# Kernel tuning notes

Measured on AMD Instinct MI355X. Metric: run time of the kernel, lower is better.

The kernel has to match this reference:

```python
import jax, jax.numpy as jnp
import numpy as np

N = 8192   # nodes per graph
F = 128    # input feature dim
H = 512    # GAT hidden dim
D = 256    # GAT output dim (== match_size, required by matching broadcast)
MS = 256   # match_size
E = 131072 # edges per graph (one direction)
EPS = 1e-8 # torch cosine_similarity eps


def _xavier(k, shape):
    lim = (6.0 / (shape[0] + shape[-1])) ** 0.5
    return jax.random.uniform(k, shape, jnp.float32, -lim, lim)


def setup_inputs() -> dict:
    key = jax.random.key(0)
    ks = jax.random.split(key, 24)
    return {
        "x_s": jax.random.normal(ks[0], (N, F), jnp.float32),
        "x_t": jax.random.normal(ks[1], (N, F), jnp.float32),
        "edge_index_s": jax.random.randint(ks[2], (2, E), 0, N),
        "edge_index_t": jax.random.randint(ks[3], (2, E), 0, N),
        "label": jax.random.randint(ks[4], (1,), 0, 2),
        # GAT params (2 single-head layers)
        "W_g1": _xavier(ks[5], (F, H)),
        "a1_src": _xavier(ks[6], (H, 1))[:, 0],
        "a1_dst": _xavier(ks[7], (H, 1))[:, 0],
        "W_g2": _xavier(ks[8], (H, D)),
        "a2_src": _xavier(ks[9], (D, 1))[:, 0],
        "a2_dst": _xavier(ks[10], (D, 1))[:, 0],
        # readout_rep
        "W_read": _xavier(ks[11], (D, D)),
        # matching
        "W_match": _xavier(ks[12], (D, MS)),
        # MLP
        "mlp_w1": _xavier(ks[13], (MS * 8, MS * 2)), "mlp_b1": jnp.zeros((MS * 2,), jnp.float32),
        "mlp_w2": _xavier(ks[14], (MS * 2, MS)),     "mlp_b2": jnp.zeros((MS,), jnp.float32),
        "mlp_w3": _xavier(ks[15], (MS, MS // 2)),    "mlp_b3": jnp.zeros((MS // 2,), jnp.float32),
        "mlp_w4": _xavier(ks[16], (MS // 2, 1)),     "mlp_b4": jnp.zeros((1,), jnp.float32),
    }


def _gat_layer(h_in, src, dst, W, a_s, a_d, n):
    h = h_in @ W                                           # [n, d_out]
    logits = (h[src] * a_s).sum(-1) + (h[dst] * a_d).sum(-1)
    e = jax.nn.leaky_relu(logits, 0.2)
    m = jax.ops.segment_max(e, dst, num_segments=n)
    ex = jnp.exp(e - m[dst])
    den = jax.ops.segment_sum(ex, dst, num_segments=n)
    alpha = ex / (den[dst] + 1e-16)
    return jax.ops.segment_sum(alpha[:, None] * h[src], dst, num_segments=n)


def _gat(x, edge_index, W1, a1s, a1d, W2, a2s, a2d):
    n = x.shape[0]
    sl = jnp.arange(n)
    # symmetrize undirected edge list + add self loops (PyG GATConv convention)
    src = jnp.concatenate([edge_index[0], edge_index[1], sl])
    dst = jnp.concatenate([edge_index[1], edge_index[0], sl])
    h = jax.nn.elu(_gat_layer(x, src, dst, W1, a1s, a1d, n))
    return _gat_layer(h, src, dst, W2, a2s, a2d, n)


def _readout(h, W):
    g = jnp.tanh(jnp.mean(h, 0) @ W)                       # [d]
    s = jax.nn.sigmoid(h @ g)                              # [n]
    return (s[:, None] * h).sum(0, keepdims=True)          # [1, d]


def _match(h1, h2, Wm):
    # cosine over feature dim of (h * W) without materializing [N, D, MS]:
    # dot[n,m] = sum_d h1[n,d]*W[d,m]*h2[n,d]*W[d,m] = ((h1*h2) @ W^2)[n,m]
    W2 = Wm * Wm
    dot = (h1 * h2) @ W2
    n1 = jnp.sqrt((h1 * h1) @ W2)
    n2 = jnp.sqrt((h2 * h2) @ W2)
    return dot / jnp.maximum(n1 * n2, EPS)


def _mutual(h1, h2):
    n1 = jnp.linalg.norm(h1, axis=-1)
    n2 = jnp.linalg.norm(h2, axis=-1)
    cos = (h1 @ h2.T) / jnp.maximum(n1[:, None] * n2[None, :], EPS)  # [N, M]
    coe = cos / cos.sum(0)                                 # column-normalize
    return coe @ h2


def _mlp(z, w1, b1, w2, b2, w3, b3, w4, b4):
    z = jax.nn.relu(z @ w1 + b1)
    z = jax.nn.relu(z @ w2 + b2)
    z = jax.nn.relu(z @ w3 + b3)
    return jax.nn.sigmoid(z @ w4 + b4)


def _forward(x_s, x_t, edge_index_s, edge_index_t, label,
             W_g1, a1_src, a1_dst, W_g2, a2_src, a2_dst,
             W_read, W_match,
             mlp_w1, mlp_b1, mlp_w2, mlp_b2, mlp_w3, mlp_b3, mlp_w4, mlp_b4):
    f1 = (x_s - jnp.mean(x_s)) / jnp.std(x_s, ddof=1)
    f2 = (x_t - jnp.mean(x_t)) / jnp.std(x_t, ddof=1)

    h1 = _gat(f1, edge_index_s, W_g1, a1_src, a1_dst, W_g2, a2_src, a2_dst)
    h2 = _gat(f2, edge_index_t, W_g1, a1_src, a1_dst, W_g2, a2_src, a2_dst)

    h1g = _readout(h1, W_read)
    h2g = _readout(h2, W_read)

    h1m = _mutual(h1, h2)
    h2m = _mutual(h2, h1)
    h1mg = _readout(h1m, W_read)
    h2mg = _readout(h2m, W_read)

    miu1 = _match(h1, h1m, W_match); miu2 = _match(h2, h2m, W_match)
    miu1g = _readout(miu1, W_read);  miu2g = _readout(miu2, W_read)
    phi1 = _match(h1, h1mg, W_match); phi2 = _match(h2, h2mg, W_match)
    phi1g = _readout(phi1, W_read);   phi2g = _readout(phi2, W_read)
    psi1 = _match(h1g, h1m, W_match); psi2 = _match(h2g, h2m, W_match)
    psi1g = _readout(psi1, W_read);   psi2g = _readout(psi2, W_read)
    om1 = _match(h1g, h1mg, W_match); om2 = _match(h2g, h2mg, W_match)

    z1 = jnp.concatenate([miu1g, phi1g, psi1g, om1], axis=1).T  # [4*MS, 1]
    z2 = jnp.concatenate([miu2g, phi2g, psi2g, om2], axis=1).T
    z = jnp.concatenate([z1, z2], axis=0).T                     # [1, 8*MS]
    z = _mlp(z, mlp_w1, mlp_b1, mlp_w2, mlp_b2, mlp_w3, mlp_b3, mlp_w4, mlp_b4)
    return z


def reference(x_s, x_t, edge_index_s, edge_index_t, label,
              W_g1, a1_src, a1_dst, W_g2, a2_src, a2_dst,
              W_read, W_match,
              mlp_w1, mlp_b1, mlp_w2, mlp_b2, mlp_w3, mlp_b3, mlp_w4, mlp_b4):
    z = _forward(x_s, x_t, edge_index_s, edge_index_t, label,
                 W_g1, a1_src, a1_dst, W_g2, a2_src, a2_dst, W_read, W_match,
                 mlp_w1, mlp_b1, mlp_w2, mlp_b2, mlp_w3, mlp_b3, mlp_w4, mlp_b4)
    label_exp = jnp.exp(-label.astype(jnp.float32))
    return z, label, label_exp
```

## Files before the change

kernel.cpp:

```cpp
#include <hip/hip_runtime.h>
#include <hip/hip_bf16.h>
#include <math.h>
#include <stddef.h>

#define NN 8192
#define FF 128
#define HH 512
#define DDIM 256
#define EE 131072
#define ET (2*EE + NN)
#define FEPS 1e-8f

typedef float f32x4 __attribute__((ext_vector_type(4)));
typedef __bf16 bf16x8 __attribute__((ext_vector_type(8)));
typedef unsigned short u16;

static __device__ __forceinline__ u16 f2bf(float f) {
  union { float f; unsigned u; } v; v.f = f;
  return (u16)((v.u + 0x7fffu + ((v.u >> 16) & 1u)) >> 16);
}
static __device__ __forceinline__ float bf2f(u16 h) {
  union { unsigned u; float f; } v; v.u = ((unsigned)h) << 16;
  return v.f;
}
static __device__ __forceinline__ f32x4 mfma16(bf16x8 a, bf16x8 b, f32x4 c) {
  return __builtin_amdgcn_mfma_f32_16x16x32_bf16(a, b, c, 0, 0, 0);
}

struct PLB { const u16* p[6]; int slot[6]; };

__global__ void k_reduce2(const float* __restrict__ xa, const float* __restrict__ xb,
                          int n, double* __restrict__ out) {
  const float* x = blockIdx.y ? xb : xa;
  double* o = out + 2 * blockIdx.y;
  __shared__ double s1[256], s2[256];
  double a = 0.0, b = 0.0;
  for (int i = blockIdx.x * blockDim.x + threadIdx.x; i < n; i += gridDim.x * blockDim.x) {
    double v = (double)x[i];
    a += v; b += v * v;
  }
  s1[threadIdx.x] = a; s2[threadIdx.x] = b;
  __syncthreads();
  for (int w = 128; w > 0; w >>= 1) {
    if (threadIdx.x < w) { s1[threadIdx.x] += s1[threadIdx.x + w]; s2[threadIdx.x] += s2[threadIdx.x + w]; }
    __syncthreads();
  }
  if (threadIdx.x == 0) { atomicAdd(&o[0], s1[0]); atomicAdd(&o[1], s2[0]); }
}

__global__ void k_normalize2(const float* __restrict__ xa, const float* __restrict__ xb,
                             u16* __restrict__ ya, u16* __restrict__ yb, int n,
                             const double* __restrict__ s) {
  const float* x = blockIdx.y ? xb : xa;
  u16* y = blockIdx.y ? yb : ya;
  const double* sp = s + 2 * blockIdx.y;
  double mean = sp[0] / (double)n;
  double var = (sp[1] - (double)n * mean * mean) / (double)(n - 1);
  float mu = (float)mean;
  float inv = (float)(1.0 / sqrt(var));
  for (int i = blockIdx.x * blockDim.x + threadIdx.x; i < n; i += gridDim.x * blockDim.x)
    y[i] = f2bf((x[i] - mu) * inv);
}

__global__ void k_hist(const int* __restrict__ ei, int* __restrict__ deg) {
  int t = blockIdx.x * blockDim.x + threadIdx.x;
  if (t >= ET) return;
  int dst = (t < EE) ? ei[EE + t] : ((t < 2*EE) ? ei[t - EE] : (t - 2*EE));
  atomicAdd(&deg[dst], 1);
}

__global__ void k_scan(const int* __restrict__ deg, int* __restrict__ offs, int* __restrict__ cursor) {
  __shared__ int ts[256];
  int tid = threadIdx.x;
  int loc[32];
  int s = 0;
  #pragma unroll
  for (int i = 0; i < 32; ++i) { loc[i] = s; s += deg[tid * 32 + i]; }
  ts[tid] = s;
  __syncthreads();
  for (int off = 1; off < 256; off <<= 1) {
    int v = (tid >= off) ? ts[tid - off] : 0;
    __syncthreads();
    ts[tid] += v;
    __syncthreads();
  }
  int pre = ts[tid] - s;
  #pragma unroll
  for (int i = 0; i < 32; ++i) {
    int o = pre + loc[i];
    offs[tid * 32 + i] = o;
    cursor[tid * 32 + i] = o;
  }
  if (tid == 255) offs[NN] = ts[255];
}

__global__ void k_scatter(const int* __restrict__ ei, int* __restrict__ cursor, int* __restrict__ srcs) {
  int t = blockIdx.x * blockDim.x + threadIdx.x;
  if (t >= ET) return;
  int src = (t < 2*EE) ? ei[t] : (t - 2*EE);
  int dst = (t < EE) ? ei[EE + t] : ((t < 2*EE) ? ei[t - EE] : (t - 2*EE));
  int pos = atomicAdd(&cursor[dst], 1);
  srcs[pos] = src;
}

__global__ __launch_bounds__(256) void k_tr_bf16(const float* __restrict__ src, u16* __restrict__ dst,
                                                 int R, int C, int sq) {
  __shared__ float T[32][33];
  int tx = threadIdx.x & 31, ty = threadIdx.x >> 5;
  int r0 = blockIdx.y * 32, c0 = blockIdx.x * 32;
  #pragma unroll
  for (int p = 0; p < 4; ++p)
    T[ty + 8 * p][tx] = src[(size_t)(r0 + ty + 8 * p) * C + c0 + tx];
  __syncthreads();
  #pragma unroll
  for (int p = 0; p < 4; ++p) {
    float v = T[tx][ty + 8 * p];
    if (sq) v *= v;
    dst[(size_t)(c0 + ty + 8 * p) * R + r0 + tx] = f2bf(v);
  }
}

__global__ __launch_bounds__(256) void k_tr2w(const float* __restrict__ hA, const float* __restrict__ scA,
                                              u16* __restrict__ tA, u16* __restrict__ wA,
                                              const float* __restrict__ hB, const float* __restrict__ scB,
                                              u16* __restrict__ tB, u16* __restrict__ wB) {
  __shared__ float T[32][33];
  __shared__ float W[32][33];
  const float* src = blockIdx.z ? hB : hA;
  const float* sc  = blockIdx.z ? scB : scA;
  u16* dt = blockIdx.z ? tB : tA;
  u16* dw = blockIdx.z ? wB : wA;
  int tx = threadIdx.x & 31, ty = threadIdx.x >> 5;
  int r0 = blockIdx.y * 32, c0 = blockIdx.x * 32;
  #pragma unroll
  for (int p = 0; p < 4; ++p) {
    int j = r0 + ty + 8 * p;
    float v = src[(size_t)j * DDIM + c0 + tx];
    T[ty + 8 * p][tx] = v;
    W[ty + 8 * p][tx] = v * sc[j];
  }
  __syncthreads();
  #pragma unroll
  for (int p = 0; p < 4; ++p) {
    size_t o = (size_t)(c0 + ty + 8 * p) * NN + r0 + tx;
    dt[o] = f2bf(T[tx][ty + 8 * p]);
    dw[o] = f2bf(W[tx][ty + 8 * p]);
  }
}

__global__ __launch_bounds__(256) void k_gemm_bf(const u16* __restrict__ A, const u16* __restrict__ Bt,
                                                 u16* __restrict__ Cb, int K, int N,
                                                 const float* __restrict__ as_, const float* __restrict__ ad_,
                                                 float* __restrict__ hs, float* __restrict__ hd) {
  int w = threadIdx.x >> 6, l = threadIdx.x & 63, r15 = l & 15, g = l >> 4;
  int i0 = blockIdx.y * 64 + w * 16;
  int n0 = blockIdx.x * 128;
  f32x4 zero = {0.f, 0.f, 0.f, 0.f};
  f32x4 acc[8];
  #pragma unroll
  for (int n = 0; n < 8; ++n) acc[n] = zero;
  int kcN = K >> 5;
  const u16* arow = A + (size_t)(i0 + r15) * K + g * 8;
  for (int kc = 0; kc < kcN; ++kc) {
    bf16x8 a = *reinterpret_cast<const bf16x8*>(arow + kc * 32);
    #pragma unroll
    for (int n = 0; n < 8; ++n) {
      bf16x8 b = *reinterpret_cast<const bf16x8*>(Bt + (size_t)(n0 + n * 16 + r15) * K + kc * 32 + g * 8);
      acc[n] = mfma16(a, b, acc[n]);
    }
  }
  int io = i0 + g * 4;
  #pragma unroll
  for (int n = 0; n < 8; ++n) {
    int c = n0 + n * 16 + r15;
    #pragma unroll
    for (int q = 0; q < 4; ++q)
      Cb[(size_t)(io + q) * N + c] = f2bf(acc[n][q]);
  }
  if (as_) {
    float hsum[4] = {0.f, 0.f, 0.f, 0.f}, dsum[4] = {0.f, 0.f, 0.f, 0.f};
    #pragma unroll
    for (int n = 0; n < 8; ++n) {
      int c = n0 + n * 16 + r15;
      float av = as_[c], dv = ad_[c];
      #pragma unroll
      for (int q = 0; q < 4; ++q) { hsum[q] += acc[n][q] * av; dsum[q] += acc[n][q] * dv; }
    }
    #pragma unroll
    for (int q = 0; q < 4; ++q) {
      #pragma unroll
      for (int o = 1; o < 16; o <<= 1) { hsum[q] += __shfl_xor(hsum[q], o); dsum[q] += __shfl_xor(dsum[q], o); }
    }
    if (r15 == 0) {
      #pragma unroll
      for (int q = 0; q < 4; ++q) {
        atomicAdd(&hs[io + q], hsum[q]);
        atomicAdd(&hd[io + q], dsum[q]);
      }
    }
  }
}

__global__ void k_alpha(const int* __restrict__ offs, const int* __restrict__ srcs,
                        const float* __restrict__ hs, const float* __restrict__ hd,
                        float* __restrict__ alpha) {
  int wid = (blockIdx.x * blockDim.x + threadIdx.x) >> 6;
  int lane = threadIdx.x & 63;
  if (wid >= NN) return;
  int b = offs[wid], e = offs[wid + 1];
  float hdn = hd[wid];
  float m = -3.4e38f;
  for (int p = b + lane; p < e; p += 64) {
    float v = hs[srcs[p]] + hdn;
    v = v > 0.f ? v : 0.2f * v;
    alpha[p] = v;
    m = fmaxf(m, v);
  }
  #pragma unroll
  for (int o = 32; o > 0; o >>= 1) m = fmaxf(m, __shfl_xor(m, o));
  float den = 0.f;
  for (int p = b + lane; p < e; p += 64) {
    float ex = expf(alpha[p] - m);
    alpha[p] = ex;
    den += ex;
  }
  #pragma unroll
  for (int o = 32; o > 0; o >>= 1) den += __shfl_xor(den, o);
  float sc = 1.f / (den + 1e-16f);
  for (int p = b + lane; p < e; p += 64) alpha[p] *= sc;
}

__global__ __launch_bounds__(256) void k_agg3(const int* __restrict__ offs, const int* __restrict__ srcs,
                                              const float* __restrict__ alpha, const u16* __restrict__ Hb,
                                              float* __restrict__ outF, u16* __restrict__ outB,
                                              int D, int elu) {
  int wv = threadIdx.x >> 6, lane = threadIdx.x & 63;
  int n = blockIdx.x * 4 + wv;
  int b = offs[n], e = offs[n + 1];
  if (D == 512) {
    float acc[8];
    #pragma unroll
    for (int j = 0; j < 8; ++j) acc[j] = 0.f;
    const u16* base = Hb + lane * 8;
    for (int p = b; p < e; ++p) {
      float a = alpha[p];
      uint4 v = *reinterpret_cast<const uint4*>(base + (size_t)srcs[p] * 512);
      acc[0] += a * bf2f((u16)(v.x & 0xffff)); acc[1] += a * bf2f((u16)(v.x >> 16));
      acc[2] += a * bf2f((u16)(v.y & 0xffff)); acc[3] += a * bf2f((u16)(v.y >> 16));
      acc[4] += a * bf2f((u16)(v.z & 0xffff)); acc[5] += a * bf2f((u16)(v.z >> 16));
      acc[6] += a * bf2f((u16)(v.w & 0xffff)); acc[7] += a * bf2f((u16)(v.w >> 16));
    }
    ushort4 o0, o1;
    #pragma unroll
    for (int j = 0; j < 8; ++j)
      if (elu) acc[j] = acc[j] > 0.f ? acc[j] : (expf(acc[j]) - 1.f);
    o0.x = f2bf(acc[0]); o0.y = f2bf(acc[1]); o0.z = f2bf(acc[2]); o0.w = f2bf(acc[3]);
    o1.x = f2bf(acc[4]); o1.y = f2bf(acc[5]); o1.z = f2bf(acc[6]); o1.w = f2bf(acc[7]);
    u16* ob = outB + (size_t)n * 512 + lane * 8;
    *reinterpret_cast<ushort4*>(ob) = o0;
    *reinterpret_cast<ushort4*>(ob + 4) = o1;
  } else {
    float acc[4];
    #pragma unroll
    for (int j = 0; j < 4; ++j) acc[j] = 0.f;
    const u16* base = Hb + lane * 4;
    for (int p = b; p < e; ++p) {
      float a = alpha[p];
      uint2 v = *reinterpret_cast<const uint2*>(base + (size_t)srcs[p] * 256);
      acc[0] += a * bf2f((u16)(v.x & 0xffff)); acc[1] += a * bf2f((u16)(v.x >> 16));
      acc[2] += a * bf2f((u16)(v.y & 0xffff)); acc[3] += a * bf2f((u16)(v.y >> 16));
    }
    #pragma unroll
    for (int j = 0; j < 4; ++j)
      if (elu) acc[j] = acc[j] > 0.f ? acc[j] : (expf(acc[j]) - 1.f);
    if (outF) {
      float4 of = {acc[0], acc[1], acc[2], acc[3]};
      *reinterpret_cast<float4*>(outF + (size_t)n * 256 + lane * 4) = of;
    }
    ushort4 ob;
    ob.x = f2bf(acc[0]); ob.y = f2bf(acc[1]); ob.z = f2bf(acc[2]); ob.w = f2bf(acc[3]);
    *reinterpret_cast<ushort4*>(outB + (size_t)n * 256 + lane * 4) = ob;
  }
}

__global__ void k_rninv2(const float* __restrict__ h1, const float* __restrict__ h2,
                         float* __restrict__ o1, float* __restrict__ o2) {
  const float* h = blockIdx.y ? h2 : h1;
  float* o = blockIdx.y ? o2 : o1;
  int wid = (blockIdx.x * blockDim.x + threadIdx.x) >> 6;
  int lane = threadIdx.x & 63;
  if (wid >= NN) return;
  float4 v = *reinterpret_cast<const float4*>(h + (size_t)wid * DDIM + lane * 4);
  float a = v.x * v.x + v.y * v.y + v.z * v.z + v.w * v.w;
  #pragma unroll
  for (int o2_ = 32; o2_ > 0; o2_ >>= 1) a += __shfl_xor(a, o2_);
  if (!lane) o[wid] = 1.f / sqrtf(a);
}

__global__ void k_wsum(const float* __restrict__ h1, const float* __restrict__ h2,
                       const float* __restrict__ n1inv, const float* __restrict__ n2inv,
                       float* __restrict__ ut) {
  const float* h = blockIdx.y ? h2 : h1;
  const float* wv = blockIdx.y ? n2inv : n1inv;
  float* o = ut + 256 * blockIdx.y;
  int d = threadIdx.x;
  int r0 = blockIdx.x * 128;
  float acc = 0.f;
  for (int r = 0; r < 128; ++r) acc += wv[r0 + r] * h[(size_t)(r0 + r) * 256 + d];
  atomicAdd(&o[d], acc);
}

__global__ void k_rs(const float* __restrict__ h1, const float* __restrict__ h2,
                     const float* __restrict__ n1inv, const float* __restrict__ n2inv,
                     const float* __restrict__ ut, float* __restrict__ R, float* __restrict__ S) {
  const float* h  = blockIdx.y ? h2 : h1;
  const float* ni = blockIdx.y ? n2inv : n1inv;
  const float* gv = blockIdx.y ? ut : ut + 256;
  float* o = blockIdx.y ? S : R;
  int wid = (blockIdx.x * blockDim.x + threadIdx.x) >> 6;
  int lane = threadIdx.x & 63;
  if (wid >= NN) return;
  float4 v = *reinterpret_cast<const float4*>(h + (size_t)wid * 256 + lane * 4);
  float4 g4 = *reinterpret_cast<const float4*>(gv + lane * 4);
  float a = v.x * g4.x + v.y * g4.y + v.z * g4.z + v.w * g4.w;
  #pragma unroll
  for (int o2_ = 32; o2_ > 0; o2_ >>= 1) a += __shfl_xor(a, o2_);
  if (!lane) o[wid] = ni[wid] * a;
}

__global__ void k_scj(const float* __restrict__ S, const float* __restrict__ R,
                      const float* __restrict__ n1inv, const float* __restrict__ n2inv,
                      float* __restrict__ scj1, float* __restrict__ scj2) {
  int j = blockIdx.x * blockDim.x + threadIdx.x;
  if (j >= NN) return;
  scj1[j] = n2inv[j] / S[j];
  scj2[j] = n1inv[j] / R[j];
}

__global__ __launch_bounds__(256) void k_gemm_M(const u16* __restrict__ A1, const u16* __restrict__ B1,
                                                const u16* __restrict__ A2, const u16* __restrict__ B2,
                                                float* __restrict__ Mf) {
  int mat = blockIdx.z & 1, kch = blockIdx.z >> 1;
  const u16* A = mat ? A2 : A1;
  const u16* Bt = mat ? B2 : B1;
  float* C = Mf + mat * 65536;
  int w = threadIdx.x >> 6, l = threadIdx.x & 63, r15 = l & 15, g = l >> 4;
  int i0 = blockIdx.y * 64 + w * 16;
  int n0 = blockIdx.x * 128;
  f32x4 zero = {0.f, 0.f, 0.f, 0.f};
  f32x4 acc[8];
  #pragma unroll
  for (int n = 0; n < 8; ++n) acc[n] = zero;
  const u16* arow = A + (size_t)(i0 + r15) * NN + g * 8;
  for (int kc = kch * 16; kc < kch * 16 + 16; ++kc) {
    bf16x8 a = *reinterpret_cast<const bf16x8*>(arow + kc * 32);
    #pragma unroll
    for (int n = 0; n < 8; ++n) {
      bf16x8 b = *reinterpret_cast<const bf16x8*>(Bt + (size_t)(n0 + n * 16 + r15) * NN + kc * 32 + g * 8);
      acc[n] = mfma16(a, b, acc[n]);
    }
  }
  int io = i0 + g * 4;
  #pragma unroll
  for (int n = 0; n < 8; ++n) {
    int c = n0 + n * 16 + r15;
    #pragma unroll
    for (int q = 0; q < 4; ++q)
      atomicAdd(&C[(size_t)(io + q) * 256 + c], acc[n][q]);
  }
}

__global__ void k_m2bf(const float* __restrict__ Mf, u16* __restrict__ Mb) {
  size_t o = (size_t)blockIdx.y * 65536 + blockIdx.x * 256 + threadIdx.x;
  Mb[o] = f2bf(Mf[o]);
}

__global__ __launch_bounds__(256) void k_gemm_hm(const u16* __restrict__ A1, const u16* __restrict__ M1,
                                                 const float* __restrict__ s1, u16* __restrict__ O1,
                                                 const u16* __restrict__ A2, const u16* __restrict__ M2,
                                                 const float* __restrict__ s2, u16* __restrict__ O2) {
  int z = blockIdx.z;
  const u16* A = z ? A2 : A1;
  const u16* Bt = z ? M2 : M1;
  const float* sc = z ? s2 : s1;
  u16* O = z ? O2 : O1;
  int w = threadIdx.x >> 6, l = threadIdx.x & 63, r15 = l & 15, g = l >> 4;
  int i0 = blockIdx.y * 64 + w * 16;
  int n0 = blockIdx.x * 128;
  f32x4 zero = {0.f, 0.f, 0.f, 0.f};
  f32x4 acc[8];
  #pragma unroll
  for (int n = 0; n < 8; ++n) acc[n] = zero;
  const u16* arow = A + (size_t)(i0 + r15) * 256 + g * 8;
  #pragma unroll
  for (int kc = 0; kc < 8; ++kc) {
    bf16x8 a = *reinterpret_cast<const bf16x8*>(arow + kc * 32);
    #pragma unroll
    for (int n = 0; n < 8; ++n) {
      bf16x8 b = *reinterpret_cast<const bf16x8*>(Bt + (size_t)(n0 + n * 16 + r15) * 256 + kc * 32 + g * 8);
      acc[n] = mfma16(a, b, acc[n]);
    }
  }
  int io = i0 + g * 4;
  float s4[4];
  #pragma unroll
  for (int q = 0; q < 4; ++q) s4[q] = sc[io + q];
  #pragma unroll
  for (int n = 0; n < 8; ++n) {
    int c = n0 + n * 16 + r15;
    #pragma unroll
    for (int q = 0; q < 4; ++q)
      O[(size_t)(io + q) * 256 + c] = f2bf(acc[n][q] * s4[q]);
  }
}

__global__ void k_w2d(const u16* __restrict__ W2t, const float* __restrict__ ogs,
                      u16* __restrict__ W2d, float* __restrict__ yn) {
  __shared__ float red[256];
  int n = blockIdx.x, z = blockIdx.y, k = threadIdx.x;
  int map = (z == 0) ? 512 : (z == 1) ? 0 : (z == 2) ? 768 : 256;
  float y = ogs[map + k];
  float wv = bf2f(W2t[n * 256 + k]);
  W2d[z * 65536 + n * 256 + k] = f2bf(wv * y);
  red[k] = wv * y * y;
  __syncthreads();
  for (int s = 128; s > 0; s >>= 1) {
    if (k < s) red[k] += red[k + s];
    __syncthreads();
  }
  if (!k) yn[z * 256 + n] = rsqrtf(fmaxf(red[0], 1e-30f));
}

__global__ __launch_bounds__(256) void k_match5(
    const u16* __restrict__ h1b, const u16* __restrict__ h1mb,
    const u16* __restrict__ h2b, const u16* __restrict__ h2mb,
    const u16* __restrict__ W2t, const u16* __restrict__ W2dB, const float* __restrict__ ynB,
    u16* __restrict__ mb0, u16* __restrict__ mb1, u16* __restrict__ mb2,
    u16* __restrict__ mb3, u16* __restrict__ mb4, u16* __restrict__ mb5) {
  int z = blockIdx.z;
  const u16* A  = z ? h2b : h1b;
  const u16* Am = z ? h2mb : h1mb;
  const u16* Wphi = W2dB + (size_t)(z ? 2 : 0) * 65536;
  const u16* Wpsi = W2dB + (size_t)(z ? 3 : 1) * 65536;
  const float* ynphi = ynB + (z ? 512 : 0);
  const float* ynpsi = ynB + (z ? 768 : 256);
  u16* oMiu = z ? mb3 : mb0;
  u16* oPhi = z ? mb4 : mb1;
  u16* oPsi = z ? mb5 : mb2;
  int w = threadIdx.x >> 6, l = threadIdx.x & 63, r15 = l & 15, g = l >> 4;
  int i0 = blockIdx.y * 64 + w * 16;
  int n0 = blockIdx.x * 64;
  f32x4 zero = {0.f, 0.f, 0.f, 0.f};
  f32x4 aP[4], aQ[4], aU[4], aD1[4], aD2[4];
  #pragma unroll
  for (int n = 0; n < 4; ++n) { aP[n] = zero; aQ[n] = zero; aU[n] = zero; aD1[n] = zero; aD2[n] = zero; }
  size_t abase = (size_t)(i0 + r15) * 256 + g * 8;
  #pragma unroll 2
  for (int kc = 0; kc < 8; ++kc) {
    uint4 xa = *reinterpret_cast<const uint4*>(A + abase + kc * 32);
    uint4 xc = *reinterpret_cast<const uint4*>(Am + abase + kc * 32);
    bf16x8 fa = *reinterpret_cast<const bf16x8*>(&xa);
    bf16x8 fc = *reinterpret_cast<const bf16x8*>(&xc);
    bf16x8 fu, fp, fq;
    float ta, tc;
    ta = bf2f((u16)(xa.x & 0xffff)); tc = bf2f((u16)(xc.x & 0xffff));
    fu[0] = (__bf16)(ta * tc); fp[0] = (__bf16)(ta * ta); fq[0] = (__bf16)(tc * tc);
    ta = bf2f((u16)(xa.x >> 16));    tc = bf2f((u16)(xc.x >> 16));
    fu[1] = (__bf16)(ta * tc); fp[1] = (__bf16)(ta * ta); fq[1] = (__bf16)(tc * tc);
    ta = bf2f((u16)(xa.y & 0xffff)); tc = bf2f((u16)(xc.y & 0xffff));
    fu[2] = (__bf16)(ta * tc); fp[2] = (__bf16)(ta * ta); fq[2] = (__bf16)(tc * tc);
    ta = bf2f((u16)(xa.y >> 16));    tc = bf2f((u16)(xc.y >> 16));
    fu[3] = (__bf16)(ta * tc); fp[3] = (__bf16)(ta * ta); fq[3] = (__bf16)(tc * tc);
    ta = bf2f((u16)(xa.z & 0xffff)); tc = bf2f((u16)(xc.z & 0xffff));
    fu[4] = (__bf16)(ta * tc); fp[4] = (__bf16)(ta * ta); fq[4] = (__bf16)(tc * tc);
    ta = bf2f((u16)(xa.z >> 16));    tc = bf2f((u16)(xc.z >> 16));
    fu[5] = (__bf16)(ta * tc); fp[5] = (__bf16)(ta * ta); fq[5] = (__bf16)(tc * tc);
    ta = bf2f((u16)(xa.w & 0xffff)); tc = bf2f((u16)(xc.w & 0xffff));
    fu[6] = (__bf16)(ta * tc); fp[6] = (__bf16)(ta * ta); fq[6] = (__bf16)(tc * tc);
    ta = bf2f((u16)(xa.w >> 16));    tc = bf2f((u16)(xc.w >> 16));
    fu[7] = (__bf16)(ta * tc); fp[7] = (__bf16)(ta * ta); fq[7] = (__bf16)(tc * tc);
    #pragma unroll
    for (int n = 0; n < 4; ++n) {
      size_t boff = (size_t)(n0 + n * 16 + r15) * 256 + kc * 32 + g * 8;
      bf16x8 bw = *reinterpret_cast<const bf16x8*>(W2t + boff);
      aP[n] = mfma16(fp, bw, aP[n]);
      aQ[n] = mfma16(fq, bw, aQ[n]);
      aU[n] = mfma16(fu, bw, aU[n]);
      bf16x8 b1 = *reinterpret_cast<const bf16x8*>(Wphi + boff);
      aD1[n] = mfma16(fa, b1, aD1[n]);
      bf16x8 b2 = *reinterpret_cast<const bf16x8*>(Wpsi + boff);
      aD2[n] = mfma16(fc, b2, aD2[n]);
    }
  }
  int io = i0 + g * 4;
  #pragma unroll
  for (int n = 0; n < 4; ++n) {
    int c = n0 + n * 16 + r15;
    float y1 = ynphi[c], y2 = ynpsi[c];
    #pragma unroll
    for (int q = 0; q < 4; ++q) {
      float rp = rsqrtf(fmaxf(aP[n][q], 1e-30f));
      float rq = rsqrtf(fmaxf(aQ[n][q], 1e-30f));
      size_t idx = (size_t)(io + q) * 256 + c;
      oMiu[idx] = f2bf(aU[n][q] * rp * rq);
      oPhi[idx] = f2bf(aD1[n][q] * rp * y1);
      oPsi[idx] = f2bf(aD2[n][q] * rq * y2);
    }
  }
}

__global__ void k_match_g(const float* __restrict__ X1, const float* __restrict__ Y1,
                          const float* __restrict__ X2, const float* __restrict__ Y2,
                          const float* __restrict__ W2, float* __restrict__ v) {
  __shared__ float u[256], p[256], q[256];
  const float* X = blockIdx.x ? X2 : X1;
  const float* Y = blockIdx.x ? Y2 : Y1;
  float* o = v + (blockIdx.x ? 1792 : 768);
  int t = threadIdx.x;
  float xv = X[t], yv = Y[t];
  u[t] = xv * yv; p[t] = xv * xv; q[t] = yv * yv;
  __syncthreads();
  float a = 0.f, b = 0.f, c = 0.f;
  #pragma unroll 4
  for (int d = 0; d < 256; ++d) {
    float wv = W2[(size_t)d * DDIM + t];
    a += u[d] * wv; b += p[d] * wv; c += q[d] * wv;
  }
  o[t] = a / fmaxf(sqrtf(b) * sqrtf(c), FEPS);
}

__global__ void k_w2(const float* __restrict__ Wm, float* __restrict__ W2, int n) {
  int i = blockIdx.x * blockDim.x + threadIdx.x;
  if (i < n) { float v = Wm[i]; W2[i] = v * v; }
}

__global__ void k_bmu_b(PLB L, float* __restrict__ mu) {
  const u16* h = L.p[blockIdx.y];
  int d = threadIdx.x;
  int r0 = blockIdx.x * 128;
  float acc = 0.f;
  for (int r = 0; r < 128; ++r) acc += bf2f(h[(size_t)(r0 + r) * 256 + d]);
  atomicAdd(&mu[blockIdx.y * 256 + d], acc);
}

__global__ void k_bgv(const float* __restrict__ mu, const float* __restrict__ Wr,
                      float* __restrict__ g) {
  __shared__ float ls[256];
  int m = blockIdx.x, t = threadIdx.x;
  ls[t] = mu[m * 256 + t] * (1.f / (float)NN);
  __syncthreads();
  float acc = 0.f;
  #pragma unroll 4
  for (int d = 0; d < 256; ++d) acc += ls[d] * Wr[(size_t)d * 256 + t];
  g[m * 256 + t] = tanhf(acc);
}

__global__ __launch_bounds__(256) void k_bsc_b(PLB L, const float* __restrict__ g,
                                               float* __restrict__ v) {
  __shared__ __align__(16) float gs[256];
  __shared__ float sarr[32];
  int m = blockIdx.y;
  const u16* h = L.p[m];
  int t = threadIdx.x, w = t >> 6, l = t & 63;
  gs[t] = g[m * 256 + t];
  __syncthreads();
  int r0 = blockIdx.x * 32;
  float4 gv4 = reinterpret_cast<const float4*>(gs)[l];
  for (int rr = w * 8; rr < w * 8 + 8; ++rr) {
    ushort4 hv = *reinterpret_cast<const ushort4*>(h + (size_t)(r0 + rr) * 256 + l * 4);
    float dot = bf2f(hv.x) * gv4.x + bf2f(hv.y) * gv4.y + bf2f(hv.z) * gv4.z + bf2f(hv.w) * gv4.w;
    #pragma unroll
    for (int o = 32; o > 0; o >>= 1) dot += __shfl_xor(dot, o);
    if (!l) sarr[rr] = 1.f / (1.f + expf(-dot));
  }
  __syncthreads();
  float acc = 0.f;
  for (int rr = 0; rr < 32; ++rr) acc += sarr[rr] * bf2f(h[(size_t)(r0 + rr) * 256 + t]);
  atomicAdd(&v[L.slot[m] + t], acc);
}

__global__ void k_binit(const float* __restrict__ b1, const float* __restrict__ b2,
                        const float* __restrict__ b3, float* __restrict__ l1,
                        float* __restrict__ l2, float* __restrict__ l3) {
  int t = blockIdx.x * 256 + threadIdx.x;
  if (t < 512) l1[t] = b1[t];
  if (t < 256) l2[t] = b2[t];
  if (t < 128) l3[t] = b3[t];
}

__global__ void k_gemv(const float* __restrict__ vin, const float* __restrict__ w,
                       float* __restrict__ out, int K, int M, int Kc, int relu_in) {
  int m = blockIdx.x * 256 + threadIdx.x;
  if (m >= M) return;
  int k0 = blockIdx.y * Kc;
  float acc = 0.f;
  #pragma unroll 4
  for (int k = k0; k < k0 + Kc; ++k) {
    float x = vin[k];
    if (relu_in) x = fmaxf(x, 0.f);
    acc += x * w[(size_t)k * M + m];
  }
  atomicAdd(&out[m], acc);
}

__global__ void k_final(const float* __restrict__ l3, const float* __restrict__ w4,
                        const float* __restrict__ b4, const int* __restrict__ label,
                        float* __restrict__ out) {
  __shared__ float ls[128];
  int t = threadIdx.x;
  ls[t] = fmaxf(l3[t], 0.f) * w4[t];
  __syncthreads();
  for (int w = 64; w > 0; w >>= 1) { if (t < w) ls[t] += ls[t + w]; __syncthreads(); }
  if (t == 0) {
    float z = 1.f / (1.f + expf(-(ls[0] + b4[0])));
    out[0] = z;
    float lb = (float)label[0];
    out[1] = lb;
    out[2] = expf(-lb);
  }
}

extern "C" void kernel_launch(void* const* d_in, const int* in_sizes, int n_in,
                              void* d_out, int out_size, void* d_ws, size_t ws_size,
                              hipStream_t stream) {
  (void)in_sizes; (void)n_in; (void)out_size;
  const float* x_s   = (const float*)d_in[0];
  const float* x_t   = (const float*)d_in[1];
  const int*   ei_s  = (const int*)d_in[2];
  const int*   ei_t  = (const int*)d_in[3];
  const int*   label = (const int*)d_in[4];
  const float* W_g1  = (const float*)d_in[5];
  const float* a1s   = (const float*)d_in[6];
  const float* a1d   = (const float*)d_in[7];
  const float* W_g2  = (const float*)d_in[8];
  const float* a2s   = (const float*)d_in[9];
  const float* a2d   = (const float*)d_in[10];
  const float* W_read  = (const float*)d_in[11];
  const float* W_match = (const float*)d_in[12];
  const float* w1 = (const float*)d_in[13]; const float* b1 = (const float*)d_in[14];
  const float* w2 = (const float*)d_in[15]; const float* b2 = (const float*)d_in[16];
  const float* w3 = (const float*)d_in[17]; const float* b3 = (const float*)d_in[18];
  const float* w4 = (const float*)d_in[19]; const float* b4 = (const float*)d_in[20];
  float* out = (float*)d_out;

  char* base = (char*)d_ws;
  size_t off = 0;
  auto alloc = [&](size_t bytes) -> void* {
    void* pp = base + off;
    off = (off + bytes + 255) & ~(size_t)255;
    return pp;
  };
  double* dsum = (double*)alloc(4 * sizeof(double));
  u16*   hb_bf= (u16*)alloc((size_t)NN * HH * 2);
  u16*   aggb = (u16*)alloc((size_t)NN * HH * 2);
  float* h1   = (float*)alloc((size_t)NN * DDIM * 4);
  float* h2   = (float*)alloc((size_t)NN * DDIM * 4);
  u16*   f1b  = (u16*)alloc((size_t)NN * FF * 2);
  u16*   f2b  = (u16*)alloc((size_t)NN * FF * 2);
  u16*   h1b  = (u16*)alloc((size_t)NN * DDIM * 2);
  u16*   h2b  = (u16*)alloc((size_t)NN * DDIM * 2);
  u16*   h1mb = (u16*)alloc((size_t)NN * DDIM * 2);
  u16*   h2mb = (u16*)alloc((size_t)NN * DDIM * 2);
  u16*   h1t  = (u16*)alloc((size_t)NN * DDIM * 2);
  u16*   h2t  = (u16*)alloc((size_t)NN * DDIM * 2);
  u16*   wh1t = (u16*)alloc((size_t)NN * DDIM * 2);
  u16*   wh2t = (u16*)alloc((size_t)NN * DDIM * 2);
  u16*   mb0  = (u16*)alloc((size_t)NN * DDIM * 2);
  u16*   mb1  = (u16*)alloc((size_t)NN * DDIM * 2);
  u16*   mb2  = (u16*)alloc((size_t)NN * DDIM * 2);
  u16*   mb3  = (u16*)alloc((size_t)NN * DDIM * 2);
  u16*   mb4  = (u16*)alloc((size_t)NN * DDIM * 2);
  u16*   mb5  = (u16*)alloc((size_t)NN * DDIM * 2);
  float* alpha= (float*)alloc((size_t)ET * 4);
  int*   srcs = (int*)alloc((size_t)ET * 4);
  int*   deg  = (int*)alloc(NN * 4);
  int*   curs = (int*)alloc(NN * 4);
  int*   offs = (int*)alloc((NN + 1) * 4);
  float* n1inv= (float*)alloc(NN * 4);
  float* n2inv= (float*)alloc(NN * 4);
  float* Rr   = (float*)alloc(NN * 4);
  float* Ss   = (float*)alloc(NN * 4);
  float* scj1 = (float*)alloc(NN * 4);
  float* scj2 = (float*)alloc(NN * 4);
  float* hsb  = (float*)alloc(NN * 4);
  float* hdb  = (float*)alloc(NN * 4);
  float* W2   = (float*)alloc((size_t)DDIM * DDIM * 4);
  u16*   Wg1t = (u16*)alloc((size_t)HH * FF * 2);
  u16*   Wg2t = (u16*)alloc((size_t)DDIM * HH * 2);
  u16*   W2t  = (u16*)alloc((size_t)DDIM * DDIM * 2);
  u16*   W2dB = (u16*)alloc(4 * 65536 * 2);
  float* ynB  = (float*)alloc(4 * 256 * 4);
  u16*   Mb   = (u16*)alloc(2 * 65536 * 2);
  float* mug1 = (float*)alloc(4 * 256 * 4);
  float* ogs  = (float*)alloc(4 * 256 * 4);
  float* mug2 = (float*)alloc(6 * 256 * 4);
  float* v    = (float*)alloc(2048 * 4);
  float* ut   = (float*)alloc(512 * 4);
  float* Mf   = (float*)alloc(2 * 65536 * 4);
  float* g1   = (float*)alloc(4 * 256 * 4);
  float* g2   = (float*)alloc(6 * 256 * 4);
  float* l1o  = (float*)alloc(512 * 4);
  float* l2o  = (float*)alloc(256 * 4);
  float* l3o  = (float*)alloc(128 * 4);
  if (off > ws_size) return;

  float* h1g  = ogs + 0;
  float* h2g  = ogs + 256;
  float* h1mg = ogs + 512;
  float* h2mg = ogs + 768;
  const size_t zr_bytes = (4 * 256 + 4 * 256 + 6 * 256 + 2048 + 512 + 2 * 65536) * 4;

  hipMemsetAsync(dsum, 0, 4 * sizeof(double), stream);
  k_reduce2<<<dim3(1024, 2), 256, 0, stream>>>(x_s, x_t, NN * FF, dsum);
  k_normalize2<<<dim3(1024, 2), 256, 0, stream>>>(x_s, x_t, f1b, f2b, NN * FF, dsum);

  k_tr_bf16<<<dim3(HH / 32, FF / 32), 256, 0, stream>>>(W_g1, Wg1t, FF, HH, 0);
  k_tr_bf16<<<dim3(DDIM / 32, HH / 32), 256, 0, stream>>>(W_g2, Wg2t, HH, DDIM, 0);
  k_tr_bf16<<<dim3(DDIM / 32, DDIM / 32), 256, 0, stream>>>(W_match, W2t, DDIM, DDIM, 1);
  k_w2<<<dim3((DDIM * DDIM + 255) / 256), 256, 0, stream>>>(W_match, W2, DDIM * DDIM);

  auto run_gat = [&](const u16* finb, const int* ei, float* hout, u16* houtb) {
    hipMemsetAsync(deg, 0, NN * 4, stream);
    k_hist<<<dim3((ET + 255) / 256), 256, 0, stream>>>(ei, deg);
    k_scan<<<1, 256, 0, stream>>>(deg, offs, curs);
    k_scatter<<<dim3((ET + 255) / 256), 256, 0, stream>>>(ei, curs, srcs);
    hipMemsetAsync(hsb, 0, 2 * NN * 4, stream);
    k_gemm_bf<<<dim3(HH / 128, NN / 64), 256, 0, stream>>>(finb, Wg1t, hb_bf, FF, HH, a1s, a1d, hsb, hdb);
    k_alpha<<<dim3(NN / 4), 256, 0, stream>>>(offs, srcs, hsb, hdb, alpha);
    k_agg3<<<dim3(NN / 4), 256, 0, stream>>>(offs, srcs, alpha, hb_bf, nullptr, aggb, HH, 1);
    hipMemsetAsync(hsb, 0, 2 * NN * 4, stream);
    k_gemm_bf<<<dim3(DDIM / 128, NN / 64), 256, 0, stream>>>(aggb, Wg2t, hb_bf, HH, DDIM, a2s, a2d, hsb, hdb);
    k_alpha<<<dim3(NN / 4), 256, 0, stream>>>(offs, srcs, hsb, hdb, alpha);
    k_agg3<<<dim3(NN / 4), 256, 0, stream>>>(offs, srcs, alpha, hb_bf, hout, houtb, DDIM, 0);
  };
  run_gat(f1b, ei_s, h1, h1b);
  run_gat(f2b, ei_t, h2, h2b);

  k_rninv2<<<dim3(NN / 4, 2), 256, 0, stream>>>(h1, h2, n1inv, n2inv);
  hipMemsetAsync(mug1, 0, zr_bytes, stream);
  k_wsum<<<dim3(64, 2), 256, 0, stream>>>(h1, h2, n1inv, n2inv, ut);
  k_rs<<<dim3(NN / 4, 2), 256, 0, stream>>>(h1, h2, n1inv, n2inv, ut, Rr, Ss);
  k_scj<<<dim3(NN / 256), 256, 0, stream>>>(Ss, Rr, n1inv, n2inv, scj1, scj2);
  k_tr2w<<<dim3(DDIM / 32, NN / 32, 2), 256, 0, stream>>>(h2, scj1, h2t, wh2t, h1, scj2, h1t, wh1t);
  k_gemm_M<<<dim3(2, 4, 32), 256, 0, stream>>>(wh2t, h2t, wh1t, h1t, Mf);
  k_m2bf<<<dim3(256, 2), 256, 0, stream>>>(Mf, Mb);
  k_gemm_hm<<<dim3(2, 128, 2), 256, 0, stream>>>(h1b, Mb, n1inv, h1mb,
                                                 h2b, Mb + 65536, n2inv, h2mb);

  PLB g1l;
  g1l.p[0] = h1b;  g1l.slot[0] = 0;
  g1l.p[1] = h2b;  g1l.slot[1] = 256;
  g1l.p[2] = h1mb; g1l.slot[2] = 512;
  g1l.p[3] = h2mb; g1l.slot[3] = 768;
  k_bmu_b<<<dim3(64, 4), 256, 0, stream>>>(g1l, mug1);
  k_bgv<<<dim3(4), 256, 0, stream>>>(mug1, W_read, g1);
  k_bsc_b<<<dim3(256, 4), 256, 0, stream>>>(g1l, g1, ogs);

  k_w2d<<<dim3(256, 4), 256, 0, stream>>>(W2t, ogs, W2dB, ynB);
  k_match5<<<dim3(4, 128, 2), 256, 0, stream>>>(h1b, h1mb, h2b, h2mb, W2t, W2dB, ynB,
                                                mb0, mb1, mb2, mb3, mb4, mb5);
  k_match_g<<<dim3(2), 256, 0, stream>>>(h1g, h1mg, h2g, h2mg, W2, v);

  PLB g2l;
  g2l.p[0] = mb0; g2l.slot[0] = 0;
  g2l.p[1] = mb1; g2l.slot[1] = 256;
  g2l.p[2] = mb2; g2l.slot[2] = 512;
  g2l.p[3] = mb3; g2l.slot[3] = 1024;
  g2l.p[4] = mb4; g2l.slot[4] = 1280;
  g2l.p[5] = mb5; g2l.slot[5] = 1536;
  k_bmu_b<<<dim3(64, 6), 256, 0, stream>>>(g2l, mug2);
  k_bgv<<<dim3(6), 256, 0, stream>>>(mug2, W_read, g2);
  k_bsc_b<<<dim3(256, 6), 256, 0, stream>>>(g2l, g2, v);

  k_binit<<<dim3(2), 256, 0, stream>>>(b1, b2, b3, l1o, l2o, l3o);
  k_gemv<<<dim3(2, 16), 256, 0, stream>>>(v, w1, l1o, 2048, 512, 128, 0);
  k_gemv<<<dim3(1, 8), 256, 0, stream>>>(l1o, w2, l2o, 512, 256, 64, 1);
  k_gemv<<<dim3(1, 8), 256, 0, stream>>>(l2o, w3, l3o, 256, 128, 32, 1);
  k_final<<<1, 128, 0, stream>>>(l3o, w4, b4, label, out);
}
```

Measured before the change: 696.9 us.

## Aggregate GAT inputs before linear projections and precompute attention weight vectors

```diff
diff --git a/kernel.cpp b/kernel.cpp
--- a/kernel.cpp
+++ b/kernel.cpp
@@ -148,8 +148,44 @@
   }
 }
 
+__global__ void k_wa(const float* __restrict__ Wg1, const float* __restrict__ a1s,
+                     const float* __restrict__ a1d, const float* __restrict__ Wg2,
+                     const float* __restrict__ a2s, const float* __restrict__ a2d,
+                     float* __restrict__ wa) {
+  int t = threadIdx.x;
+  if (blockIdx.x == 0) {
+    if (t < 128) {
+      float s = 0.f, d = 0.f;
+      for (int j = 0; j < 512; ++j) { float w = Wg1[(size_t)t * 512 + j]; s += w * a1s[j]; d += w * a1d[j]; }
+      wa[t] = s; wa[128 + t] = d;
+    }
+  } else {
+    for (int k = t; k < 512; k += 256) {
+      float s = 0.f, d = 0.f;
+      for (int j = 0; j < 256; ++j) { float w = Wg2[(size_t)k * 256 + j]; s += w * a2s[j]; d += w * a2d[j]; }
+      wa[256 + k] = s; wa[768 + k] = d;
+    }
+  }
+}
+
+__global__ void k_dots1(const u16* __restrict__ fb, const float* __restrict__ wa,
+                        float* __restrict__ hs, float* __restrict__ hd) {
+  int wid = (blockIdx.x * blockDim.x + threadIdx.x) >> 6;
+  int lane = threadIdx.x & 63;
+  if (wid >= NN) return;
+  unsigned v = *reinterpret_cast<const unsigned*>(fb + (size_t)wid * 128 + lane * 2);
+  float f0 = bf2f((u16)(v & 0xffff)), f1 = bf2f((u16)(v >> 16));
+  float2 ws = *reinterpret_cast<const float2*>(wa + lane * 2);
+  float2 wd = *reinterpret_cast<const float2*>(wa + 128 + lane * 2);
+  float s = f0 * ws.x + f1 * ws.y;
+  float d = f0 * wd.x + f1 * wd.y;
+  #pragma unroll
+  for (int o = 32; o > 0; o >>= 1) { s += __shfl_xor(s, o); d += __shfl_xor(d, o); }
+  if (!lane) { hs[wid] = s; hd[wid] = d; }
+}
+
 __global__ __launch_bounds__(256) void k_gemm_bf(const u16* __restrict__ A, const u16* __restrict__ Bt,
-                                                 u16* __restrict__ Cb, int K, int N,
+                                                 u16* __restrict__ Cb, int K, int N, int elu,
                                                  const float* __restrict__ as_, const float* __restrict__ ad_,
                                                  float* __restrict__ hs, float* __restrict__ hd) {
   int w = threadIdx.x >> 6, l = threadIdx.x & 63, r15 = l & 15, g = l >> 4;
@@ -168,6 +204,13 @@
       bf16x8 b = *reinterpret_cast<const bf16x8*>(Bt + (size_t)(n0 + n * 16 + r15) * K + kc * 32 + g * 8);
       acc[n] = mfma16(a, b, acc[n]);
     }
+  }
+  if (elu) {
+    #pragma unroll
+    for (int n = 0; n < 8; ++n)
+      #pragma unroll
+      for (int q = 0; q < 4; ++q)
+        acc[n][q] = acc[n][q] > 0.f ? acc[n][q] : (expf(acc[n][q]) - 1.f);
   }
   int io = i0 + g * 4;
   #pragma unroll
@@ -230,57 +273,45 @@
   for (int p = b + lane; p < e; p += 64) alpha[p] *= sc;
 }
 
-__global__ __launch_bounds__(256) void k_agg3(const int* __restrict__ offs, const int* __restrict__ srcs,
-                                              const float* __restrict__ alpha, const u16* __restrict__ Hb,
-                                              float* __restrict__ outF, u16* __restrict__ outB,
-                                              int D, int elu) {
+__global__ __launch_bounds__(256) void k_aggf(const int* __restrict__ offs, const int* __restrict__ srcs,
+                                              const float* __restrict__ alpha, const u16* __restrict__ fb,
+                                              u16* __restrict__ aggout) {
   int wv = threadIdx.x >> 6, lane = threadIdx.x & 63;
   int n = blockIdx.x * 4 + wv;
   int b = offs[n], e = offs[n + 1];
-  if (D == 512) {
-    float acc[8];
-    #pragma unroll
-    for (int j = 0; j < 8; ++j) acc[j] = 0.f;
-    const u16* base = Hb + lane * 8;
-    for (int p = b; p < e; ++p) {
-      float a = alpha[p];
-      uint4 v = *reinterpret_cast<const uint4*>(base + (size_t)srcs[p] * 512);
-      acc[0] += a * bf2f((u16)(v.x & 0xffff)); acc[1] += a * bf2f((u16)(v.x >> 16));
-      acc[2] += a * bf2f((u16)(v.y & 0xffff)); acc[3] += a * bf2f((u16)(v.y >> 16));
-      acc[4] += a * bf2f((u16)(v.z & 0xffff)); acc[5] += a * bf2f((u16)(v.z >> 16));
-      acc[6] += a * bf2f((u16)(v.w & 0xffff)); acc[7] += a * bf2f((u16)(v.w >> 16));
-    }
-    ushort4 o0, o1;
-    #pragma unroll
-    for (int j = 0; j < 8; ++j)
-      if (elu) acc[j] = acc[j] > 0.f ? acc[j] : (expf(acc[j]) - 1.f);
-    o0.x = f2bf(acc[0]); o0.y = f2bf(acc[1]); o0.z = f2bf(acc[2]); o0.w = f2bf(acc[3]);
-    o1.x = f2bf(acc[4]); o1.y = f2bf(acc[5]); o1.z = f2bf(acc[6]); o1.w = f2bf(acc[7]);
-    u16* ob = outB + (size_t)n * 512 + lane * 8;
-    *reinterpret_cast<ushort4*>(ob) = o0;
-    *reinterpret_cast<ushort4*>(ob + 4) = o1;
-  } else {
-    float acc[4];
-    #pragma unroll
-    for (int j = 0; j < 4; ++j) acc[j] = 0.f;
-    const u16* base = Hb + lane * 4;
-    for (int p = b; p < e; ++p) {
-      float a = alpha[p];
-      uint2 v = *reinterpret_cast<const uint2*>(base + (size_t)srcs[p] * 256);
-      acc[0] += a * bf2f((u16)(v.x & 0xffff)); acc[1] += a * bf2f((u16)(v.x >> 16));
-      acc[2] += a * bf2f((u16)(v.y & 0xffff)); acc[3] += a * bf2f((u16)(v.y >> 16));
-    }
-    #pragma unroll
-    for (int j = 0; j < 4; ++j)
-      if (elu) acc[j] = acc[j] > 0.f ? acc[j] : (expf(acc[j]) - 1.f);
-    if (outF) {
-      float4 of = {acc[0], acc[1], acc[2], acc[3]};
-      *reinterpret_cast<float4*>(outF + (size_t)n * 256 + lane * 4) = of;
-    }
-    ushort4 ob;
-    ob.x = f2bf(acc[0]); ob.y = f2bf(acc[1]); ob.z = f2bf(acc[2]); ob.w = f2bf(acc[3]);
-    *reinterpret_cast<ushort4*>(outB + (size_t)n * 256 + lane * 4) = ob;
-  }
+  float a0 = 0.f, a1 = 0.f;
+  const u16* base = fb + lane * 2;
+  for (int p = b; p < e; ++p) {
+    float a = alpha[p];
+    unsigned v = *reinterpret_cast<const unsigned*>(base + (size_t)srcs[p] * 128);
+    a0 += a * bf2f((u16)(v & 0xffff));
+    a1 += a * bf2f((u16)(v >> 16));
+  }
+  unsigned o = ((unsigned)f2bf(a1) << 16) | (unsigned)f2bf(a0);
+  *reinterpret_cast<unsigned*>(aggout + (size_t)n * 128 + lane * 2) = o;
+}
+
+__global__ __launch_bounds__(256) void k_agg3(const int* __restrict__ offs, const int* __restrict__ srcs,
+                                              const float* __restrict__ alpha, const u16* __restrict__ Hb,
+                                              float* __restrict__ outF, u16* __restrict__ outB) {
+  int wv = threadIdx.x >> 6, lane = threadIdx.x & 63;
+  int n = blockIdx.x * 4 + wv;
+  int b = offs[n], e = offs[n + 1];
+  float acc[4];
+  #pragma unroll
+  for (int j = 0; j < 4; ++j) acc[j] = 0.f;
+  const u16* base = Hb + lane * 4;
+  for (int p = b; p < e; ++p) {
+    float a = alpha[p];
+    uint2 v = *reinterpret_cast<const uint2*>(base + (size_t)srcs[p] * 256);
+    acc[0] += a * bf2f((u16)(v.x & 0xffff)); acc[1] += a * bf2f((u16)(v.x >> 16));
+    acc[2] += a * bf2f((u16)(v.y & 0xffff)); acc[3] += a * bf2f((u16)(v.y >> 16));
+  }
+  float4 of = {acc[0], acc[1], acc[2], acc[3]};
+  *reinterpret_cast<float4*>(outF + (size_t)n * 256 + lane * 4) = of;
+  ushort4 ob;
+  ob.x = f2bf(acc[0]); ob.y = f2bf(acc[1]); ob.z = f2bf(acc[2]); ob.w = f2bf(acc[3]);
+  *reinterpret_cast<ushort4*>(outB + (size_t)n * 256 + lane * 4) = ob;
 }
 
 __global__ void k_rninv2(const float* __restrict__ h1, const float* __restrict__ h2,
@@ -431,7 +462,7 @@
   if (!k) yn[z * 256 + n] = rsqrtf(fmaxf(red[0], 1e-30f));
 }
 
-__global__ __launch_bounds__(256) void k_match5(
+__global__ __launch_bounds__(256, 2) void k_match5(
     const u16* __restrict__ h1b, const u16* __restrict__ h1mb,
     const u16* __restrict__ h2b, const u16* __restrict__ h2mb,
     const u16* __restrict__ W2t, const u16* __restrict__ W2dB, const float* __restrict__ ynB,
@@ -449,13 +480,12 @@
   u16* oPsi = z ? mb5 : mb2;
   int w = threadIdx.x >> 6, l = threadIdx.x & 63, r15 = l & 15, g = l >> 4;
   int i0 = blockIdx.y * 64 + w * 16;
-  int n0 = blockIdx.x * 64;
+  int n0 = blockIdx.x * 128;
   f32x4 zero = {0.f, 0.f, 0.f, 0.f};
-  f32x4 aP[4], aQ[4], aU[4], aD1[4], aD2[4];
-  #pragma unroll
-  for (int n = 0; n < 4; ++n) { aP[n] = zero; aQ[n] = zero; aU[n] = zero; aD1[n] = zero; aD2[n] = zero; }
+  f32x4 aP[8], aQ[8], aU[8], aD1[8], aD2[8];
+  #pragma unroll
+  for (int n = 0; n < 8; ++n) { aP[n] = zero; aQ[n] = zero; aU[n] = zero; aD1[n] = zero; aD2[n] = zero; }
   size_t abase = (size_t)(i0 + r15) * 256 + g * 8;
-  #pragma unroll 2
   for (int kc = 0; kc < 8; ++kc) {
     uint4 xa = *reinterpret_cast<const uint4*>(A + abase + kc * 32);
     uint4 xc = *reinterpret_cast<const uint4*>(Am + abase + kc * 32);
@@ -480,7 +510,7 @@
     ta = bf2f((u16)(xa.w >> 16));    tc = bf2f((u16)(xc.w >> 16));
     fu[7] = (__bf16)(ta * tc); fp[7] = (__bf16)(ta * ta); fq[7] = (__bf16)(tc * tc);
     #pragma unroll
-    for (int n = 0; n < 4; ++n) {
+    for (int n = 0; n < 8; ++n) {
       size_t boff = (size_t)(n0 + n * 16 + r15) * 256 + kc * 32 + g * 8;
       bf16x8 bw = *reinterpret_cast<const bf16x8*>(W2t + boff);
       aP[n] = mfma16(fp, bw, aP[n]);
@@ -494,7 +524,7 @@
   }
   int io = i0 + g * 4;
   #pragma unroll
-  for (int n = 0; n < 4; ++n) {
+  for (int n = 0; n < 8; ++n) {
     int c = n0 + n * 16 + r15;
     float y1 = ynphi[c], y2 = ynpsi[c];
     #pragma unroll
@@ -651,8 +681,9 @@
     return pp;
   };
   double* dsum = (double*)alloc(4 * sizeof(double));
-  u16*   hb_bf= (u16*)alloc((size_t)NN * HH * 2);
-  u16*   aggb = (u16*)alloc((size_t)NN * HH * 2);
+  u16*   gb   = (u16*)alloc((size_t)NN * HH * 2);
+  u16*   h2pb = (u16*)alloc((size_t)NN * DDIM * 2);
+  u16*   aggfb= (u16*)alloc((size_t)NN * FF * 2);
   float* h1   = (float*)alloc((size_t)NN * DDIM * 4);
   float* h2   = (float*)alloc((size_t)NN * DDIM * 4);
   u16*   f1b  = (u16*)alloc((size_t)NN * FF * 2);
@@ -691,6 +722,7 @@
   u16*   W2dB = (u16*)alloc(4 * 65536 * 2);
   float* ynB  = (float*)alloc(4 * 256 * 4);
   u16*   Mb   = (u16*)alloc(2 * 65536 * 2);
+  float* wa   = (float*)alloc(1280 * 4);
   float* mug1 = (float*)alloc(4 * 256 * 4);
   float* ogs  = (float*)alloc(4 * 256 * 4);
   float* mug2 = (float*)alloc(6 * 256 * 4);
@@ -718,20 +750,23 @@
   k_tr_bf16<<<dim3(DDIM / 32, HH / 32), 256, 0, stream>>>(W_g2, Wg2t, HH, DDIM, 0);
   k_tr_bf16<<<dim3(DDIM / 32, DDIM / 32), 256, 0, stream>>>(W_match, W2t, DDIM, DDIM, 1);
   k_w2<<<dim3((DDIM * DDIM + 255) / 256), 256, 0, stream>>>(W_match, W2, DDIM * DDIM);
+  k_wa<<<dim3(2), 256, 0, stream>>>(W_g1, a1s, a1d, W_g2, a2s, a2d, wa);
 
   auto run_gat = [&](const u16* finb, const int* ei, float* hout, u16* houtb) {
     hipMemsetAsync(deg, 0, NN * 4, stream);
     k_hist<<<dim3((ET + 255) / 256), 256, 0, stream>>>(ei, deg);
     k_scan<<<1, 256, 0, stream>>>(deg, offs, curs);
     k_scatter<<<dim3((ET + 255) / 256), 256, 0, stream>>>(ei, curs, srcs);
+    k_dots1<<<dim3(NN / 4), 256, 0, stream>>>(finb, wa, hsb, hdb);
+    k_alpha<<<dim3(NN / 4), 256, 0, stream>>>(offs, srcs, hsb, hdb, alpha);
+    k_aggf<<<dim3(NN / 4), 256, 0, stream>>>(offs, srcs, alpha, finb, aggfb);
     hipMemsetAsync(hsb, 0, 2 * NN * 4, stream);
-    k_gemm_bf<<<dim3(HH / 128, NN / 64), 256, 0, stream>>>(finb, Wg1t, hb_bf, FF, HH, a1s, a1d, hsb, hdb);
+    k_gemm_bf<<<dim3(HH / 128, NN / 64), 256, 0, stream>>>(aggfb, Wg1t, gb, FF, HH, 1,
+                                                           wa + 256, wa + 768, hsb, hdb);
     k_alpha<<<dim3(NN / 4), 256, 0, stream>>>(offs, srcs, hsb, hdb, alpha);
-    k_agg3<<<dim3(NN / 4), 256, 0, stream>>>(offs, srcs, alpha, hb_bf, nullptr, aggb, HH, 1);
-    hipMemsetAsync(hsb, 0, 2 * NN * 4, stream);
-    k_gemm_bf<<<dim3(DDIM / 128, NN / 64), 256, 0, stream>>>(aggb, Wg2t, hb_bf, HH, DDIM, a2s, a2d, hsb, hdb);
-    k_alpha<<<dim3(NN / 4), 256, 0, stream>>>(offs, srcs, hsb, hdb, alpha);
-    k_agg3<<<dim3(NN / 4), 256, 0, stream>>>(offs, srcs, alpha, hb_bf, hout, houtb, DDIM, 0);
+    k_gemm_bf<<<dim3(DDIM / 128, NN / 64), 256, 0, stream>>>(gb, Wg2t, h2pb, HH, DDIM, 0,
+                                                             nullptr, nullptr, nullptr, nullptr);
+    k_agg3<<<dim3(NN / 4), 256, 0, stream>>>(offs, srcs, alpha, h2pb, hout, houtb);
   };
   run_gat(f1b, ei_s, h1, h1b);
   run_gat(f2b, ei_t, h2, h2b);
@@ -757,7 +792,7 @@
   k_bsc_b<<<dim3(256, 4), 256, 0, stream>>>(g1l, g1, ogs);
 
   k_w2d<<<dim3(256, 4), 256, 0, stream>>>(W2t, ogs, W2dB, ynB);
-  k_match5<<<dim3(4, 128, 2), 256, 0, stream>>>(h1b, h1mb, h2b, h2mb, W2t, W2dB, ynB,
+  k_match5<<<dim3(2, 128, 2), 256, 0, stream>>>(h1b, h1mb, h2b, h2mb, W2t, W2dB, ynB,
                                                 mb0, mb1, mb2, mb3, mb4, mb5);
   k_match_g<<<dim3(2), 256, 0, stream>>>(h1g, h1mg, h2g, h2mg, W2, v);
 
```

Measured after the change: 682.1 us. 2.1% less time.
